# Performance work log

Hardware: AMD Instinct MI355X
Metric: run time of the kernel (lower is better)

The kernel has to match this reference:

```python
import jax, jax.numpy as jnp
import numpy as np

B, S, HID = 4, 1024, 2048
NH, NKV = 32, 8
HD = HID // NH  # 64
N_REP = NH // NKV
THETA = 10000.0


def _rope_cos_sin(position_ids, head_dim, dtype):
    inv_freq = 1.0 / (THETA ** (jnp.arange(0, head_dim, 2, dtype=jnp.float32) / head_dim))
    ang = position_ids.astype(jnp.float32)[:, None] * inv_freq[None, :]  # [S, HD/2]
    emb = jnp.concatenate([ang, ang], axis=-1)  # [S, HD]
    return jnp.cos(emb).astype(dtype), jnp.sin(emb).astype(dtype)


def _rotate_half(x):
    x1, x2 = jnp.split(x, 2, axis=-1)
    return jnp.concatenate([-x2, x1], axis=-1)


def setup_inputs() -> dict:
    key = jax.random.key(0)
    ks = jax.random.split(key, 6)
    scale = 0.02
    hidden_states = jax.random.normal(ks[0], (B, S, HID), dtype=jnp.float32)
    # causal additive mask
    neg = jnp.finfo(jnp.float32).min
    causal = jnp.where(jnp.tril(jnp.ones((S, S), dtype=bool)), 0.0, neg)
    attention_mask = causal[None, None, :, :].astype(jnp.float32)
    position_ids = jnp.arange(S, dtype=jnp.int32)
    Wq = jax.random.normal(ks[1], (HID, NH * HD), dtype=jnp.float32) * scale
    Wk = jax.random.normal(ks[2], (HID, NKV * HD), dtype=jnp.float32) * scale
    Wv = jax.random.normal(ks[3], (HID, NKV * HD), dtype=jnp.float32) * scale
    Wo = jax.random.normal(ks[4], (NH * HD, HID), dtype=jnp.float32) * scale
    return {"hidden_states": hidden_states, "attention_mask": attention_mask,
            "position_ids": position_ids, "Wq": Wq, "Wk": Wk, "Wv": Wv, "Wo": Wo}


def reference(hidden_states, attention_mask, position_ids, Wq, Wk, Wv, Wo):
    b, s, _ = hidden_states.shape
    dtype = hidden_states.dtype
    q = (hidden_states @ Wq).reshape(b, s, NH, HD).transpose(0, 2, 1, 3)   # [B,NH,S,HD]
    k = (hidden_states @ Wk).reshape(b, s, NKV, HD).transpose(0, 2, 1, 3)  # [B,NKV,S,HD]
    v = (hidden_states @ Wv).reshape(b, s, NKV, HD).transpose(0, 2, 1, 3)
    # RoPE
    cos, sin = _rope_cos_sin(position_ids, HD, dtype)  # [S,HD]
    cos = cos[None, None, :, :]
    sin = sin[None, None, :, :]
    q = q * cos + _rotate_half(q) * sin
    k = k * cos + _rotate_half(k) * sin
    # repeat KV heads to match query heads
    k = jnp.repeat(k, N_REP, axis=1)  # [B,NH,S,HD]
    v = jnp.repeat(v, N_REP, axis=1)
    scale = HD ** -0.5
    attn = jnp.einsum('bhqd,bhkd->bhqk', q, k) * scale + attention_mask
    attn = jax.nn.softmax(attn.astype(jnp.float32), axis=-1).astype(dtype)
    out = jnp.einsum('bhqk,bhkd->bhqd', attn, v)  # [B,NH,S,HD]
    out = out.transpose(0, 2, 1, 3).reshape(b, s, NH * HD)
    return out @ Wo
```

## Files before the change

### kernel.cpp

```cpp
#include <hip/hip_runtime.h>
#include <hip/hip_bf16.h>
#include <math.h>

typedef __bf16 bf16_t;
typedef __bf16 bf16x4 __attribute__((ext_vector_type(4)));
typedef __bf16 bf16x8 __attribute__((ext_vector_type(8)));
typedef float f32x4 __attribute__((ext_vector_type(4)));

#define MFMA_BF16(a, b, c) __builtin_amdgcn_mfma_f32_16x16x32_bf16((a), (b), (c), 0, 0, 0)

__device__ __forceinline__ void gload_lds16(const void* g, void* s) {
  __builtin_amdgcn_global_load_lds((const __attribute__((address_space(1))) void*)g,
                                   (__attribute__((address_space(3))) void*)s, 16, 0, 0);
}

__device__ __forceinline__ bf16x8 lds_frag(const bf16_t* base, int row, int k) {
  const char* p = reinterpret_cast<const char*>(base) + row * 128 + ((((k >> 3) ^ (row & 7)) << 4));
  return *reinterpret_cast<const bf16x8*>(p);
}

__global__ __launch_bounds__(256) void k_cvt_x(const float* __restrict__ X, bf16_t* __restrict__ Xb) {
  const int i = blockIdx.x * 256 + threadIdx.x;
  const float4* X4 = reinterpret_cast<const float4*>(X);
  const float4 a = X4[2 * i], c = X4[2 * i + 1];
  bf16x8 v;
  v[0] = (bf16_t)a.x; v[1] = (bf16_t)a.y; v[2] = (bf16_t)a.z; v[3] = (bf16_t)a.w;
  v[4] = (bf16_t)c.x; v[5] = (bf16_t)c.y; v[6] = (bf16_t)c.z; v[7] = (bf16_t)c.w;
  reinterpret_cast<bf16x8*>(Xb)[i] = v;
}

__global__ __launch_bounds__(256) void k_transpose(const float* __restrict__ W, bf16_t* __restrict__ Wt,
                                                   int K, int N) {
  __shared__ bf16_t t[64][65];
  const int k0 = blockIdx.y * 64, n0 = blockIdx.x * 64;
  const int tid = threadIdx.x;
#pragma unroll
  for (int i = 0; i < 16; ++i) {
    const int idx = i * 256 + tid;
    const int kl = idx >> 6, nl = idx & 63;
    t[nl][kl] = (bf16_t)W[(size_t)(k0 + kl) * N + n0 + nl];
  }
  __syncthreads();
#pragma unroll
  for (int i = 0; i < 16; ++i) {
    const int idx = i * 256 + tid;
    const int nl = idx >> 6, kl = idx & 63;
    Wt[(size_t)(n0 + nl) * K + k0 + kl] = t[nl][kl];
  }
}

__global__ __launch_bounds__(256) void k_transpose_qkv(const float* __restrict__ Wq,
                                                       const float* __restrict__ Wk,
                                                       const float* __restrict__ Wv,
                                                       bf16_t* __restrict__ Wt) {
  __shared__ bf16_t t[64][65];
  const int n0 = blockIdx.x * 64;
  const int k0 = blockIdx.y * 64;
  const int tid = threadIdx.x;
  const float* W;
  int N, nbase;
  if (n0 < 2048)      { W = Wq; N = 2048; nbase = 0; }
  else if (n0 < 2560) { W = Wk; N = 512;  nbase = 2048; }
  else                { W = Wv; N = 512;  nbase = 2560; }
  const int nl0 = n0 - nbase;
#pragma unroll
  for (int i = 0; i < 16; ++i) {
    const int idx = i * 256 + tid;
    const int kl = idx >> 6, nl = idx & 63;
    t[nl][kl] = (bf16_t)W[(size_t)(k0 + kl) * N + nl0 + nl];
  }
  __syncthreads();
#pragma unroll
  for (int i = 0; i < 16; ++i) {
    const int idx = i * 256 + tid;
    const int nl = idx >> 6, kl = idx & 63;
    Wt[(size_t)(n0 + nl) * 2048 + k0 + kl] = t[nl][kl];
  }
}

__global__ __launch_bounds__(512) void k_gemm_qkv(const bf16_t* __restrict__ A,
                                                  const bf16_t* __restrict__ Bt,
                                                  const int* __restrict__ pos_ids,
                                                  bf16_t* __restrict__ Qb,
                                                  bf16_t* __restrict__ Kb,
                                                  bf16_t* __restrict__ Vt) {
  constexpr int K = 2048;
  constexpr int NT = K / 64;
  __shared__ __align__(16) char smem[131072];
  const int tid = threadIdx.x;
  const int w = tid >> 6, l = tid & 63;
  const int wm = w >> 2, wn = w & 3;
  const int g = l >> 4, ln = l & 15;
  const int orig = blockIdx.y * 12 + blockIdx.x;
  const int swz = (orig & 7) * 24 + (orig >> 3);
  const int m0 = (swz / 12) * 256, n0 = (swz % 12) * 256;
  const int csrc = ((l & 7) ^ (l >> 3)) * 8;
  const int srow = w * 16 + (l >> 3);

  auto STAGE_A = [&](int slot, int h, int kt) {
    char* base = smem + slot * 32768 + h * 16384 + w * 2048;
    const bf16_t* gs = A + (size_t)(m0 + h * 128 + srow) * K + kt + csrc;
    gload_lds16(gs, base);
    gload_lds16(gs + (size_t)8 * K, base + 1024);
  };
  auto STAGE_B = [&](int slot, int h, int kt) {
    char* base = smem + 65536 + slot * 32768 + h * 16384 + w * 2048;
    const bf16_t* gs = Bt + (size_t)(n0 + h * 128 + srow) * K + kt + csrc;
    gload_lds16(gs, base);
    gload_lds16(gs + (size_t)8 * K, base + 1024);
  };
  auto FRAG = [&](const char* half, int row, int kk) -> bf16x8 {
    return *reinterpret_cast<const bf16x8*>(half + row * 128 + ((((kk >> 3) ^ (row & 7)) << 4)));
  };

  const f32x4 zero4 = {0.f, 0.f, 0.f, 0.f};
  f32x4 acc[8][4];
#pragma unroll
  for (int i = 0; i < 8; ++i)
#pragma unroll
    for (int j = 0; j < 4; ++j) acc[i][j] = zero4;

  STAGE_A(0, 0, 0); STAGE_A(0, 1, 0);
  STAGE_B(0, 0, 0); STAGE_B(0, 1, 0);
  STAGE_B(1, 0, 64); STAGE_B(1, 1, 64);
  asm volatile("s_waitcnt vmcnt(4)" ::: "memory");
  __builtin_amdgcn_sched_barrier(0);
  __builtin_amdgcn_s_barrier();
  __builtin_amdgcn_sched_barrier(0);

  const int rb = (wn & 1) * 64;
  for (int t = 0; t < NT; ++t) {
    const int s = t & 1;
    const char* Ah = smem + s * 32768 + wm * 16384;
    const char* Bh = smem + 65536 + s * 32768 + (wn >> 1) * 16384;
    bf16x8 bB[4][2];
#pragma unroll
    for (int q = 0; q < 4; ++q) {
      if (q == 0) {
#pragma unroll
        for (int fc = 0; fc < 4; ++fc)
#pragma unroll
          for (int kh = 0; kh < 2; ++kh) bB[fc][kh] = FRAG(Bh, rb + fc * 16 + ln, kh * 32 + g * 8);
      }
      bf16x8 aA[2][2];
#pragma unroll
      for (int e = 0; e < 2; ++e)
#pragma unroll
        for (int kh = 0; kh < 2; ++kh) aA[e][kh] = FRAG(Ah, (q * 2 + e) * 16 + ln, kh * 32 + g * 8);
      if (q == 0 && t + 1 < NT) STAGE_A(s ^ 1, 0, (t + 1) * 64);
      if (q == 1 && t + 1 < NT) STAGE_A(s ^ 1, 1, (t + 1) * 64);
      if (q == 2 && t + 2 < NT) STAGE_B(s, 0, (t + 2) * 64);
      if (q == 3 && t + 2 < NT) STAGE_B(s, 1, (t + 2) * 64);
      if (q == 3) {
        if (t >= NT - 2) asm volatile("s_waitcnt vmcnt(0)" ::: "memory");
        else             asm volatile("s_waitcnt vmcnt(4)" ::: "memory");
      }
      __builtin_amdgcn_sched_barrier(0);
      __builtin_amdgcn_s_barrier();
      __builtin_amdgcn_sched_barrier(0);
      __builtin_amdgcn_s_setprio(1);
#pragma unroll
      for (int e = 0; e < 2; ++e)
#pragma unroll
        for (int fc = 0; fc < 4; ++fc)
#pragma unroll
          for (int kh = 0; kh < 2; ++kh)
            acc[q * 2 + e][fc] = MFMA_BF16(aA[e][kh], bB[fc][kh], acc[q * 2 + e][fc]);
      __builtin_amdgcn_s_setprio(0);
      __builtin_amdgcn_sched_barrier(0);
      __builtin_amdgcn_s_barrier();
      __builtin_amdgcn_sched_barrier(0);
    }
  }

  const int colbase = n0 + wn * 64;
  const int rowbase = m0 + wm * 128;
  const float if0 = exp2f(-(float)ln * 0.4152410118609203f);
  const float if1 = exp2f(-(float)(ln + 16) * 0.4152410118609203f);
  const float QS = 0.125f * 1.4426950408889634f;

  if (colbase < 2560) {
    const bool isQ = (colbase < 2048);
    bf16_t* out = isQ ? (Qb + (size_t)(colbase >> 6) * 1024 * 64)
                      : (Kb + (size_t)((colbase - 2048) >> 6) * 1024 * 64);
    const size_t bstride = isQ ? (size_t)32 * 1024 * 64 : (size_t)8 * 1024 * 64;
    const float sc = isQ ? QS : 1.0f;
#pragma unroll
    for (int i = 0; i < 8; ++i)
#pragma unroll
      for (int r = 0; r < 4; ++r) {
        const int row = rowbase + i * 16 + g * 4 + r;
        const int b = row >> 10, s = row & 1023;
        const float pos = (float)pos_ids[s];
        float sn0, cs0, sn1, cs1;
        __sincosf(pos * if0, &sn0, &cs0);
        __sincosf(pos * if1, &sn1, &cs1);
        const float x0 = acc[i][0][r], x1 = acc[i][1][r];
        const float x2 = acc[i][2][r], x3 = acc[i][3][r];
        const float o0 = (x0 * cs0 - x2 * sn0) * sc;
        const float o2 = (x2 * cs0 + x0 * sn0) * sc;
        const float o1 = (x1 * cs1 - x3 * sn1) * sc;
        const float o3 = (x3 * cs1 + x1 * sn1) * sc;
        bf16_t* p = out + (size_t)b * bstride + (size_t)s * 64;
        p[ln] = (bf16_t)o0;
        p[16 + ln] = (bf16_t)o1;
        p[32 + ln] = (bf16_t)o2;
        p[48 + ln] = (bf16_t)o3;
      }
  } else {
    const int kh = (colbase - 2560) >> 6;
#pragma unroll
    for (int i = 0; i < 8; ++i)
#pragma unroll
      for (int r = 0; r < 4; ++r) {
        const int row = rowbase + i * 16 + g * 4 + r;
        const int b = row >> 10, s = row & 1023;
        const size_t vb = ((size_t)(b * 8 + kh) * 64) * 1024;
#pragma unroll
        for (int j = 0; j < 4; ++j) {
          const int d = j * 16 + ln;
          Vt[vb + (size_t)d * 1024 + s] = (bf16_t)acc[i][j][r];
        }
      }
  }
}

__global__ __launch_bounds__(512) void k_gemm2(const bf16_t* __restrict__ A,
                                               const bf16_t* __restrict__ Bt,
                                               float* __restrict__ C) {
  constexpr int K = 2048;
  constexpr int NT = K / 64;
  constexpr int N = 2048;
  __shared__ __align__(16) char smem[98304];
  const int tid = threadIdx.x;
  const int w = tid >> 6, l = tid & 63;
  const int g = l >> 4, ln = l & 15;
  const int orig = blockIdx.y * 8 + blockIdx.x;
  const int swz = (orig & 7) * 32 + (orig >> 3);
  const int m0 = (swz >> 3) * 128, n0 = (swz & 7) * 256;
  const int csrc = ((l & 7) ^ (l >> 3)) * 8;
  const int srow = w * 16 + (l >> 3);

  auto STAGE_A = [&](int slot, int kt) {
    char* base = smem + slot * 16384 + w * 2048;
    const bf16_t* gs = A + (size_t)(m0 + srow) * K + kt + csrc;
    gload_lds16(gs, base);
    gload_lds16(gs + (size_t)8 * K, base + 1024);
  };
  auto STAGE_B = [&](int slot, int h, int kt) {
    char* base = smem + 32768 + slot * 32768 + h * 16384 + w * 2048;
    const bf16_t* gs = Bt + (size_t)(n0 + h * 128 + srow) * K + kt + csrc;
    gload_lds16(gs, base);
    gload_lds16(gs + (size_t)8 * K, base + 1024);
  };
  auto FRAG = [&](const char* half, int row, int kk) -> bf16x8 {
    return *reinterpret_cast<const bf16x8*>(half + row * 128 + ((((kk >> 3) ^ (row & 7)) << 4)));
  };

  const f32x4 zero4 = {0.f, 0.f, 0.f, 0.f};
  f32x4 acc[8][2];
#pragma unroll
  for (int i = 0; i < 8; ++i)
#pragma unroll
    for (int j = 0; j < 2; ++j) acc[i][j] = zero4;

  STAGE_A(0, 0);
  STAGE_B(0, 0, 0); STAGE_B(0, 1, 0);
  STAGE_B(1, 0, 64); STAGE_B(1, 1, 64);
  asm volatile("s_waitcnt vmcnt(4)" ::: "memory");
  __builtin_amdgcn_sched_barrier(0);
  __builtin_amdgcn_s_barrier();
  __builtin_amdgcn_sched_barrier(0);

  const int brow = w * 32;
  for (int t = 0; t < NT; ++t) {
    const int s = t & 1;
    const char* Ah = smem + s * 16384;
    const char* Bh = smem + 32768 + s * 32768 + (brow >> 7) * 16384;
    const int rb = brow & 127;
    bf16x8 bB[2][2];
#pragma unroll
    for (int q = 0; q < 4; ++q) {
      if (q == 0) {
#pragma unroll
        for (int fc = 0; fc < 2; ++fc)
#pragma unroll
          for (int kh = 0; kh < 2; ++kh) bB[fc][kh] = FRAG(Bh, rb + fc * 16 + ln, kh * 32 + g * 8);
      }
      bf16x8 aA[2][2];
#pragma unroll
      for (int e = 0; e < 2; ++e)
#pragma unroll
        for (int kh = 0; kh < 2; ++kh) aA[e][kh] = FRAG(Ah, (q * 2 + e) * 16 + ln, kh * 32 + g * 8);
      if (q == 0 && t + 1 < NT) STAGE_A(s ^ 1, (t + 1) * 64);
      if (q == 1 && t + 2 < NT) STAGE_B(s, 0, (t + 2) * 64);
      if (q == 2 && t + 2 < NT) STAGE_B(s, 1, (t + 2) * 64);
      if (q == 3) {
        if (t >= NT - 2) asm volatile("s_waitcnt vmcnt(0)" ::: "memory");
        else             asm volatile("s_waitcnt vmcnt(4)" ::: "memory");
      }
      __builtin_amdgcn_sched_barrier(0);
      __builtin_amdgcn_s_barrier();
      __builtin_amdgcn_sched_barrier(0);
      __builtin_amdgcn_s_setprio(1);
#pragma unroll
      for (int e = 0; e < 2; ++e)
#pragma unroll
        for (int fc = 0; fc < 2; ++fc)
#pragma unroll
          for (int kh = 0; kh < 2; ++kh)
            acc[q * 2 + e][fc] = MFMA_BF16(aA[e][kh], bB[fc][kh], acc[q * 2 + e][fc]);
      __builtin_amdgcn_s_setprio(0);
      __builtin_amdgcn_sched_barrier(0);
      __builtin_amdgcn_s_barrier();
      __builtin_amdgcn_sched_barrier(0);
    }
  }

#pragma unroll
  for (int i = 0; i < 8; ++i)
#pragma unroll
    for (int fc = 0; fc < 2; ++fc)
#pragma unroll
      for (int r = 0; r < 4; ++r) {
        const int row = m0 + i * 16 + g * 4 + r;
        const int col = n0 + brow + fc * 16 + ln;
        C[(size_t)row * N + col] = acc[i][fc][r];
      }
}

__global__ __launch_bounds__(256) void k_attn(const bf16_t* __restrict__ Qb,
                                              const bf16_t* __restrict__ Kb,
                                              const bf16_t* __restrict__ Vt,
                                              bf16_t* __restrict__ AO) {
  __shared__ bf16_t Ks[2][64 * 64];
  __shared__ bf16_t Vs[2][64 * 64];
  __shared__ bf16_t Ps[4][16 * 64];
  const int tid = threadIdx.x;
  const int w = tid >> 6, l = tid & 63;
  const int g = l >> 4, ln = l & 15;
  const int lr = l >> 3;
  const int csrc = ((l & 7) ^ lr) * 8;
  const int f = blockIdx.x;
  const int bh = blockIdx.y;
  const int b = bh >> 5, h = bh & 31, kh = h >> 2;
  const int qA0 = f * 64, qB0 = (15 - f) * 64;
  const int qAw = qA0 + w * 16, qBw = qB0 + w * 16;
  const bf16_t* Qh = Qb + (size_t)(b * 32 + h) * 1024 * 64;
  const bf16_t* Kh = Kb + (size_t)(b * 8 + kh) * 1024 * 64;
  const bf16_t* Vh = Vt + (size_t)(b * 8 + kh) * 64 * 1024;

  bf16x8 aqA[2], aqB[2];
  aqA[0] = *reinterpret_cast<const bf16x8*>(Qh + (size_t)(qAw + ln) * 64 + g * 8);
  aqA[1] = *reinterpret_cast<const bf16x8*>(Qh + (size_t)(qAw + ln) * 64 + 32 + g * 8);
  aqB[0] = *reinterpret_cast<const bf16x8*>(Qh + (size_t)(qBw + ln) * 64 + g * 8);
  aqB[1] = *reinterpret_cast<const bf16x8*>(Qh + (size_t)(qBw + ln) * 64 + 32 + g * 8);

  const f32x4 zero4 = {0.f, 0.f, 0.f, 0.f};
  f32x4 oA[4], oB[4];
#pragma unroll
  for (int d = 0; d < 4; ++d) { oA[d] = zero4; oB[d] = zero4; }
  float lA[4], lB[4];
#pragma unroll
  for (int r = 0; r < 4; ++r) { lA[r] = 0.f; lB[r] = 0.f; }

  auto STAGE = [&](int buf, int kt) {
#pragma unroll
    for (int c = 0; c < 2; ++c) {
      const int cq = c * 4 + w;
      const int r = cq * 8 + lr;
      gload_lds16(Kh + (size_t)(kt * 64 + r) * 64 + csrc, &Ks[buf][cq * 512]);
      gload_lds16(Vh + (size_t)r * 1024 + kt * 64 + csrc, &Vs[buf][cq * 512]);
    }
  };

  auto ACT = [&](const bf16x8 (&aq)[2], f32x4 (&o)[4], float (&lr_)[4],
                 int qw0, bool dg, int kt, const bf16_t* Kc, const bf16_t* Vc) {
    f32x4 sc[4];
#pragma unroll
    for (int nb = 0; nb < 4; ++nb) {
      const bf16x8 k0 = lds_frag(Kc, nb * 16 + ln, g * 8);
      const bf16x8 k1 = lds_frag(Kc, nb * 16 + ln, 32 + g * 8);
      f32x4 z = zero4;
      z = MFMA_BF16(aq[0], k0, z);
      sc[nb] = MFMA_BF16(aq[1], k1, z);
    }
#pragma unroll
    for (int r = 0; r < 4; ++r) {
      const int qrow = qw0 + g * 4 + r;
      float rs = 0.f;
#pragma unroll
      for (int nb = 0; nb < 4; ++nb) {
        float v = sc[nb][r];
        if (dg && (kt * 64 + nb * 16 + ln) > qrow) v = -INFINITY;
        const float p = exp2f(v - 16.0f);
        sc[nb][r] = p;
        rs += p;
      }
      lr_[r] += rs;
    }

    char* pw = reinterpret_cast<char*>(&Ps[w][0]);
#pragma unroll
    for (int r = 0; r < 4; ++r) {
      const int q = g * 4 + r;
      const int sw = (q & 7) << 4;
#pragma unroll
      for (int nb = 0; nb < 4; ++nb) {
        const int byte = q * 128 + ((nb * 16 + ln) * 2);
        *reinterpret_cast<bf16_t*>(pw + (byte ^ sw)) = (bf16_t)sc[nb][r];
      }
    }
    asm volatile("s_waitcnt lgkmcnt(0)" ::: "memory");

    const bf16x8 pa0 = lds_frag(&Ps[w][0], ln, g * 8);
    const bf16x8 pa1 = lds_frag(&Ps[w][0], ln, 32 + g * 8);
#pragma unroll
    for (int d = 0; d < 4; ++d) {
      const bf16x8 v0 = lds_frag(Vc, d * 16 + ln, g * 8);
      const bf16x8 v1 = lds_frag(Vc, d * 16 + ln, 32 + g * 8);
      o[d] = MFMA_BF16(pa0, v0, o[d]);
      o[d] = MFMA_BF16(pa1, v1, o[d]);
    }
  };

  const int nA = f + 1;
  STAGE(0, 0);

  for (int t = 0; t < 17; ++t) {
    const int cur = t & 1;
    asm volatile("s_waitcnt vmcnt(0)" ::: "memory");
    __syncthreads();
    if (t + 1 < 17) {
      const int ktn = (t + 1 < nA) ? (t + 1) : (t + 1 - nA);
      STAGE(cur ^ 1, ktn);
    }
    const bf16_t* Kc = &Ks[cur][0];
    const bf16_t* Vc = &Vs[cur][0];
    if (t < nA) ACT(aqA, oA, lA, qAw, t == nA - 1, t, Kc, Vc);
    else        ACT(aqB, oB, lB, qBw, t == 16, t - nA, Kc, Vc);
  }

  auto EPI = [&](f32x4 (&o)[4], float (&lr_)[4], int qw0) {
#pragma unroll
    for (int r = 0; r < 4; ++r) {
      float rs = lr_[r];
      rs += __shfl_xor(rs, 1);
      rs += __shfl_xor(rs, 2);
      rs += __shfl_xor(rs, 4);
      rs += __shfl_xor(rs, 8);
      const float inv = 1.0f / rs;
      const int srow = qw0 + g * 4 + r;
      const size_t base = ((size_t)(b * 1024 + srow)) * 2048 + h * 64;
#pragma unroll
      for (int d = 0; d < 4; ++d) AO[base + d * 16 + ln] = (bf16_t)(o[d][r] * inv);
    }
  };
  EPI(oA, lA, qAw);
  EPI(oB, lB, qBw);
}

extern "C" void kernel_launch(void* const* d_in, const int* in_sizes, int n_in,
                              void* d_out, int out_size, void* d_ws, size_t ws_size,
                              hipStream_t stream) {
  const float* X = (const float*)d_in[0];
  const int* pos = (const int*)d_in[2];
  const float* Wq = (const float*)d_in[3];
  const float* Wk = (const float*)d_in[4];
  const float* Wv = (const float*)d_in[5];
  const float* Wo = (const float*)d_in[6];
  float* out = (float*)d_out;
  char* ws = (char*)d_ws;

  bf16_t* Xb   = (bf16_t*)(ws);
  bf16_t* Wqkv = (bf16_t*)(ws + 16777216);
  bf16_t* Wot  = (bf16_t*)(ws + 29360128);
  bf16_t* Qb   = (bf16_t*)(ws + 62914560);
  bf16_t* Kb   = (bf16_t*)(ws + 79691776);
  bf16_t* Vt   = (bf16_t*)(ws + 83886080);
  bf16_t* AO   = (bf16_t*)(ws + 37748736);

  k_cvt_x<<<4096, 256, 0, stream>>>(X, Xb);
  k_transpose_qkv<<<dim3(48, 32), 256, 0, stream>>>(Wq, Wk, Wv, Wqkv);
  k_transpose<<<dim3(32, 32), 256, 0, stream>>>(Wo, Wot, 2048, 2048);
  k_gemm_qkv<<<dim3(12, 16), 512, 0, stream>>>(Xb, Wqkv, pos, Qb, Kb, Vt);
  k_attn<<<dim3(8, 128), 256, 0, stream>>>(Qb, Kb, Vt, AO);
  k_gemm2<<<dim3(8, 32), 512, 0, stream>>>(AO, Wot, out);
}
```

Baseline: 176.1 us.

## Retile QKV GEMM to 256x192 tiles with triple-buffered B and fold softmax shift

The QKV projection GEMM moves from 256x256 tiles (192 blocks) to 256x192 tiles (256 blocks), so the grid fills all 256 CUs of the MI355X. Each wave now owns 32 rows by all 192 columns, and B tiles are triple-buffered in a larger LDS allocation. The epilogue is restructured per 64-column head group. Separately, the attention kernel folds the constant -16 softmax shift into the MFMA accumulator initial value, which removes a subtraction per score.

```diff
diff --git a/kernel.cpp b/kernel.cpp
--- a/kernel.cpp
+++ b/kernel.cpp
@@ -86,142 +86,145 @@
                                                   bf16_t* __restrict__ Vt) {
   constexpr int K = 2048;
   constexpr int NT = K / 64;
-  __shared__ __align__(16) char smem[131072];
+  __shared__ __align__(16) char smem[139264];
   const int tid = threadIdx.x;
   const int w = tid >> 6, l = tid & 63;
-  const int wm = w >> 2, wn = w & 3;
   const int g = l >> 4, ln = l & 15;
-  const int orig = blockIdx.y * 12 + blockIdx.x;
-  const int swz = (orig & 7) * 24 + (orig >> 3);
-  const int m0 = (swz / 12) * 256, n0 = (swz % 12) * 256;
+  const int orig = blockIdx.y * 16 + blockIdx.x;
+  const int swz = (orig & 7) * 32 + (orig >> 3);
+  const int m0 = (swz >> 4) * 256, n0 = (swz & 15) * 192;
   const int csrc = ((l & 7) ^ (l >> 3)) * 8;
-  const int srow = w * 16 + (l >> 3);
-
-  auto STAGE_A = [&](int slot, int h, int kt) {
-    char* base = smem + slot * 32768 + h * 16384 + w * 2048;
-    const bf16_t* gs = A + (size_t)(m0 + h * 128 + srow) * K + kt + csrc;
+  const int rowbase = m0 + w * 32;
+
+  auto STAGE_A = [&](int slot, int half, int kt) {
+    char* base = smem + slot * 32768 + w * 4096 + half * 2048;
+    const bf16_t* gs = A + (size_t)(m0 + w * 32 + half * 16 + (l >> 3)) * K + kt + csrc;
     gload_lds16(gs, base);
     gload_lds16(gs + (size_t)8 * K, base + 1024);
   };
-  auto STAGE_B = [&](int slot, int h, int kt) {
-    char* base = smem + 65536 + slot * 32768 + h * 16384 + w * 2048;
-    const bf16_t* gs = Bt + (size_t)(n0 + h * 128 + srow) * K + kt + csrc;
+  auto STAGE_B = [&](int slot, int j, int kt) {
+    char* base = smem + 65536 + slot * 24576 + w * 3072 + j * 1024;
+    const bf16_t* gs = Bt + (size_t)(n0 + w * 24 + j * 8 + (l >> 3)) * K + kt + csrc;
     gload_lds16(gs, base);
-    gload_lds16(gs + (size_t)8 * K, base + 1024);
-  };
-  auto FRAG = [&](const char* half, int row, int kk) -> bf16x8 {
-    return *reinterpret_cast<const bf16x8*>(half + row * 128 + ((((kk >> 3) ^ (row & 7)) << 4)));
+  };
+  auto FRAG = [&](const char* base, int row, int kk) -> bf16x8 {
+    return *reinterpret_cast<const bf16x8*>(base + row * 128 + ((((kk >> 3) ^ (row & 7)) << 4)));
   };
 
   const f32x4 zero4 = {0.f, 0.f, 0.f, 0.f};
-  f32x4 acc[8][4];
-#pragma unroll
-  for (int i = 0; i < 8; ++i)
-#pragma unroll
-    for (int j = 0; j < 4; ++j) acc[i][j] = zero4;
+  f32x4 acc[2][12];
+#pragma unroll
+  for (int i = 0; i < 2; ++i)
+#pragma unroll
+    for (int j = 0; j < 12; ++j) acc[i][j] = zero4;
 
   STAGE_A(0, 0, 0); STAGE_A(0, 1, 0);
-  STAGE_B(0, 0, 0); STAGE_B(0, 1, 0);
-  STAGE_B(1, 0, 64); STAGE_B(1, 1, 64);
-  asm volatile("s_waitcnt vmcnt(4)" ::: "memory");
+  STAGE_B(0, 0, 0); STAGE_B(0, 1, 0); STAGE_B(0, 2, 0);
+  STAGE_B(1, 0, 64); STAGE_B(1, 1, 64); STAGE_B(1, 2, 64);
+  asm volatile("s_waitcnt vmcnt(3)" ::: "memory");
   __builtin_amdgcn_sched_barrier(0);
   __builtin_amdgcn_s_barrier();
   __builtin_amdgcn_sched_barrier(0);
 
-  const int rb = (wn & 1) * 64;
   for (int t = 0; t < NT; ++t) {
-    const int s = t & 1;
-    const char* Ah = smem + s * 32768 + wm * 16384;
-    const char* Bh = smem + 65536 + s * 32768 + (wn >> 1) * 16384;
-    bf16x8 bB[4][2];
+    const int as = t & 1;
+    const int bs = t % 3;
+    const int bs2 = (t + 2) % 3;
+    const char* Abase = smem + as * 32768;
+    const char* Bbase = smem + 65536 + bs * 24576;
+    bf16x8 aA[2][2];
 #pragma unroll
     for (int q = 0; q < 4; ++q) {
       if (q == 0) {
 #pragma unroll
-        for (int fc = 0; fc < 4; ++fc)
-#pragma unroll
-          for (int kh = 0; kh < 2; ++kh) bB[fc][kh] = FRAG(Bh, rb + fc * 16 + ln, kh * 32 + g * 8);
-      }
-      bf16x8 aA[2][2];
+        for (int e = 0; e < 2; ++e)
+#pragma unroll
+          for (int kh = 0; kh < 2; ++kh)
+            aA[e][kh] = FRAG(Abase, w * 32 + e * 16 + ln, kh * 32 + g * 8);
+      }
+      bf16x8 bB[3][2];
+#pragma unroll
+      for (int fc = 0; fc < 3; ++fc)
+#pragma unroll
+        for (int kh = 0; kh < 2; ++kh)
+          bB[fc][kh] = FRAG(Bbase, (q * 3 + fc) * 16 + ln, kh * 32 + g * 8);
+      if (q == 0 && t + 1 < NT) STAGE_A(as ^ 1, 0, (t + 1) * 64);
+      if (q == 1 && t + 1 < NT) STAGE_A(as ^ 1, 1, (t + 1) * 64);
+      if (q == 2 && t + 2 < NT) { STAGE_B(bs2, 0, (t + 2) * 64); STAGE_B(bs2, 1, (t + 2) * 64); }
+      if (q == 3) {
+        if (t + 2 < NT) STAGE_B(bs2, 2, (t + 2) * 64);
+        if (t >= NT - 2) asm volatile("s_waitcnt vmcnt(0)" ::: "memory");
+        else             asm volatile("s_waitcnt vmcnt(3)" ::: "memory");
+      }
+      __builtin_amdgcn_sched_barrier(0);
+      __builtin_amdgcn_s_barrier();
+      __builtin_amdgcn_sched_barrier(0);
+      __builtin_amdgcn_s_setprio(1);
 #pragma unroll
       for (int e = 0; e < 2; ++e)
 #pragma unroll
-        for (int kh = 0; kh < 2; ++kh) aA[e][kh] = FRAG(Ah, (q * 2 + e) * 16 + ln, kh * 32 + g * 8);
-      if (q == 0 && t + 1 < NT) STAGE_A(s ^ 1, 0, (t + 1) * 64);
-      if (q == 1 && t + 1 < NT) STAGE_A(s ^ 1, 1, (t + 1) * 64);
-      if (q == 2 && t + 2 < NT) STAGE_B(s, 0, (t + 2) * 64);
-      if (q == 3 && t + 2 < NT) STAGE_B(s, 1, (t + 2) * 64);
-      if (q == 3) {
-        if (t >= NT - 2) asm volatile("s_waitcnt vmcnt(0)" ::: "memory");
-        else             asm volatile("s_waitcnt vmcnt(4)" ::: "memory");
-      }
+        for (int fc = 0; fc < 3; ++fc)
+#pragma unroll
+          for (int kh = 0; kh < 2; ++kh)
+            acc[e][q * 3 + fc] = MFMA_BF16(aA[e][kh], bB[fc][kh], acc[e][q * 3 + fc]);
+      __builtin_amdgcn_s_setprio(0);
       __builtin_amdgcn_sched_barrier(0);
       __builtin_amdgcn_s_barrier();
       __builtin_amdgcn_sched_barrier(0);
-      __builtin_amdgcn_s_setprio(1);
-#pragma unroll
-      for (int e = 0; e < 2; ++e)
-#pragma unroll
-        for (int fc = 0; fc < 4; ++fc)
-#pragma unroll
-          for (int kh = 0; kh < 2; ++kh)
-            acc[q * 2 + e][fc] = MFMA_BF16(aA[e][kh], bB[fc][kh], acc[q * 2 + e][fc]);
-      __builtin_amdgcn_s_setprio(0);
-      __builtin_amdgcn_sched_barrier(0);
-      __builtin_amdgcn_s_barrier();
-      __builtin_amdgcn_sched_barrier(0);
-    }
-  }
-
-  const int colbase = n0 + wn * 64;
-  const int rowbase = m0 + wm * 128;
+    }
+  }
+
   const float if0 = exp2f(-(float)ln * 0.4152410118609203f);
   const float if1 = exp2f(-(float)(ln + 16) * 0.4152410118609203f);
   const float QS = 0.125f * 1.4426950408889634f;
 
-  if (colbase < 2560) {
-    const bool isQ = (colbase < 2048);
-    bf16_t* out = isQ ? (Qb + (size_t)(colbase >> 6) * 1024 * 64)
-                      : (Kb + (size_t)((colbase - 2048) >> 6) * 1024 * 64);
-    const size_t bstride = isQ ? (size_t)32 * 1024 * 64 : (size_t)8 * 1024 * 64;
-    const float sc = isQ ? QS : 1.0f;
-#pragma unroll
-    for (int i = 0; i < 8; ++i)
-#pragma unroll
-      for (int r = 0; r < 4; ++r) {
-        const int row = rowbase + i * 16 + g * 4 + r;
-        const int b = row >> 10, s = row & 1023;
-        const float pos = (float)pos_ids[s];
-        float sn0, cs0, sn1, cs1;
-        __sincosf(pos * if0, &sn0, &cs0);
-        __sincosf(pos * if1, &sn1, &cs1);
-        const float x0 = acc[i][0][r], x1 = acc[i][1][r];
-        const float x2 = acc[i][2][r], x3 = acc[i][3][r];
-        const float o0 = (x0 * cs0 - x2 * sn0) * sc;
-        const float o2 = (x2 * cs0 + x0 * sn0) * sc;
-        const float o1 = (x1 * cs1 - x3 * sn1) * sc;
-        const float o3 = (x3 * cs1 + x1 * sn1) * sc;
-        bf16_t* p = out + (size_t)b * bstride + (size_t)s * 64;
-        p[ln] = (bf16_t)o0;
-        p[16 + ln] = (bf16_t)o1;
-        p[32 + ln] = (bf16_t)o2;
-        p[48 + ln] = (bf16_t)o3;
-      }
-  } else {
-    const int kh = (colbase - 2560) >> 6;
-#pragma unroll
-    for (int i = 0; i < 8; ++i)
-#pragma unroll
-      for (int r = 0; r < 4; ++r) {
-        const int row = rowbase + i * 16 + g * 4 + r;
-        const int b = row >> 10, s = row & 1023;
-        const size_t vb = ((size_t)(b * 8 + kh) * 64) * 1024;
-#pragma unroll
-        for (int j = 0; j < 4; ++j) {
-          const int d = j * 16 + ln;
-          Vt[vb + (size_t)d * 1024 + s] = (bf16_t)acc[i][j][r];
+#pragma unroll
+  for (int gg = 0; gg < 3; ++gg) {
+    const int colg = n0 + gg * 64;
+    if (colg < 2560) {
+      const bool isQ = (colg < 2048);
+      bf16_t* out = isQ ? (Qb + (size_t)(colg >> 6) * 1024 * 64)
+                        : (Kb + (size_t)((colg - 2048) >> 6) * 1024 * 64);
+      const size_t bstride = isQ ? (size_t)32 * 1024 * 64 : (size_t)8 * 1024 * 64;
+      const float sc = isQ ? QS : 1.0f;
+#pragma unroll
+      for (int i = 0; i < 2; ++i)
+#pragma unroll
+        for (int r = 0; r < 4; ++r) {
+          const int row = rowbase + i * 16 + g * 4 + r;
+          const int b = row >> 10, s = row & 1023;
+          const float pos = (float)pos_ids[s];
+          float sn0, cs0, sn1, cs1;
+          __sincosf(pos * if0, &sn0, &cs0);
+          __sincosf(pos * if1, &sn1, &cs1);
+          const float x0 = acc[i][gg * 4 + 0][r], x1 = acc[i][gg * 4 + 1][r];
+          const float x2 = acc[i][gg * 4 + 2][r], x3 = acc[i][gg * 4 + 3][r];
+          const float o0 = (x0 * cs0 - x2 * sn0) * sc;
+          const float o2 = (x2 * cs0 + x0 * sn0) * sc;
+          const float o1 = (x1 * cs1 - x3 * sn1) * sc;
+          const float o3 = (x3 * cs1 + x1 * sn1) * sc;
+          bf16_t* p = out + (size_t)b * bstride + (size_t)s * 64;
+          p[ln] = (bf16_t)o0;
+          p[16 + ln] = (bf16_t)o1;
+          p[32 + ln] = (bf16_t)o2;
+          p[48 + ln] = (bf16_t)o3;
         }
-      }
+    } else {
+      const int kh = (colg - 2560) >> 6;
+#pragma unroll
+      for (int i = 0; i < 2; ++i)
+#pragma unroll
+        for (int r = 0; r < 4; ++r) {
+          const int row = rowbase + i * 16 + g * 4 + r;
+          const int b = row >> 10, s = row & 1023;
+          const size_t vb = ((size_t)(b * 8 + kh) * 64) * 1024;
+#pragma unroll
+          for (int fcl = 0; fcl < 4; ++fcl) {
+            const int d = fcl * 16 + ln;
+            Vt[vb + (size_t)d * 1024 + s] = (bf16_t)acc[i][gg * 4 + fcl][r];
+          }
+        }
+    }
   }
 }
 
@@ -357,6 +360,7 @@
   aqB[1] = *reinterpret_cast<const bf16x8*>(Qh + (size_t)(qBw + ln) * 64 + 32 + g * 8);
 
   const f32x4 zero4 = {0.f, 0.f, 0.f, 0.f};
+  const f32x4 shift4 = {-16.f, -16.f, -16.f, -16.f};
   f32x4 oA[4], oB[4];
 #pragma unroll
   for (int d = 0; d < 4; ++d) { oA[d] = zero4; oB[d] = zero4; }
@@ -381,7 +385,7 @@
     for (int nb = 0; nb < 4; ++nb) {
       const bf16x8 k0 = lds_frag(Kc, nb * 16 + ln, g * 8);
       const bf16x8 k1 = lds_frag(Kc, nb * 16 + ln, 32 + g * 8);
-      f32x4 z = zero4;
+      f32x4 z = shift4;
       z = MFMA_BF16(aq[0], k0, z);
       sc[nb] = MFMA_BF16(aq[1], k1, z);
     }
@@ -393,7 +397,7 @@
       for (int nb = 0; nb < 4; ++nb) {
         float v = sc[nb][r];
         if (dg && (kt * 64 + nb * 16 + ln) > qrow) v = -INFINITY;
-        const float p = exp2f(v - 16.0f);
+        const float p = exp2f(v);
         sc[nb][r] = p;
         rs += p;
       }
@@ -483,7 +487,7 @@
   k_cvt_x<<<4096, 256, 0, stream>>>(X, Xb);
   k_transpose_qkv<<<dim3(48, 32), 256, 0, stream>>>(Wq, Wk, Wv, Wqkv);
   k_transpose<<<dim3(32, 32), 256, 0, stream>>>(Wo, Wot, 2048, 2048);
-  k_gemm_qkv<<<dim3(12, 16), 512, 0, stream>>>(Xb, Wqkv, pos, Qb, Kb, Vt);
+  k_gemm_qkv<<<dim3(16, 16), 512, 0, stream>>>(Xb, Wqkv, pos, Qb, Kb, Vt);
   k_attn<<<dim3(8, 128), 256, 0, stream>>>(Qb, Kb, Vt, AO);
   k_gemm2<<<dim3(8, 32), 512, 0, stream>>>(AO, Wot, out);
 }
```

New measurement: 170.3 us. 1.03x faster.
